# Kernel optimization log

Hardware: AMD Instinct MI355X
Metric: run time of the kernel (lower is better)

## Reference

```python
import jax, jax.numpy as jnp
import numpy as np

N = 50000          # nodes
E = 400000         # edges
MUL = 32           # multiplicity per irrep
NUM_NEIGHBORS = 8.0
INV_SQRT3 = 1.0 / np.sqrt(3.0)  # w3j(1,1,0) coefficient


def setup_inputs() -> dict:
    key = jax.random.key(0)
    ks = jax.random.split(key, 20)
    inp = {
        # node_input: 32x0e (dim 32) + 32x1o (dim 96) = 128
        "node_input": jax.random.normal(ks[0], (N, 4 * MUL), jnp.float32),
        "node_attr": jnp.ones((N, 1), jnp.float32),           # 1x0e trivial attr
        "edge_src": jax.random.randint(ks[1], (E,), 0, N, jnp.int32),
        "edge_dst": jax.random.randint(ks[2], (E,), 0, N, jnp.int32),
        "edge_attr": jax.random.normal(ks[3], (E, 4), jnp.float32),   # 1x0e + 1x1o
        "edge_scalars": jax.random.normal(ks[4], (E, 16), jnp.float32),
        # FullyConnectedTensorProduct weights (uvw, node_attr has mul 1)
        "w_sc0": jax.random.normal(ks[5], (MUL, MUL), jnp.float32),
        "w_sc1": jax.random.normal(ks[6], (MUL, MUL), jnp.float32),
        "w_lin1_0": jax.random.normal(ks[7], (MUL, MUL), jnp.float32),
        "w_lin1_1": jax.random.normal(ks[8], (MUL, MUL), jnp.float32),
        # radial FC net -> per-edge TP weights (numel = 4*MUL = 128)
        "fc_w1": jax.random.normal(ks[9], (16, 64), jnp.float32),
        "fc_w2": jax.random.normal(ks[10], (64, 4 * MUL), jnp.float32),
        # lin2: irreps_mid (64x0e+64x1o) x attr -> output
        "w_lin2_0": jax.random.normal(ks[11], (2 * MUL, MUL), jnp.float32),
        "w_lin2_1": jax.random.normal(ks[12], (2 * MUL, MUL), jnp.float32),
        # alpha: irreps_mid x attr -> 0e (zero-init in original; small randn for a nontrivial test)
        "w_alpha": 0.1 * jax.random.normal(ks[13], (2 * MUL, 1), jnp.float32),
        # sc_edges: irreps_mid x edge_attr -> edge_attr
        "w_se0a": jax.random.normal(ks[14], (2 * MUL,), jnp.float32),  # mid0e x ea0e -> 0e
        "w_se0b": jax.random.normal(ks[15], (2 * MUL,), jnp.float32),  # mid1o x ea1o -> 0e
        "w_se1a": jax.random.normal(ks[16], (2 * MUL,), jnp.float32),  # mid0e x ea1o -> 1o
        "w_se1b": jax.random.normal(ks[17], (2 * MUL,), jnp.float32),  # mid1o x ea0e -> 1o
    }
    return inp


def reference(node_input, node_attr, edge_src, edge_dst, edge_attr, edge_scalars,
              w_sc0, w_sc1, w_lin1_0, w_lin1_1, fc_w1, fc_w2,
              w_lin2_0, w_lin2_1, w_alpha, w_se0a, w_se0b, w_se1a, w_se1b):
    inv_nn = 1.0 / jnp.sqrt(jnp.asarray(NUM_NEIGHBORS, node_input.dtype))
    n = node_input.shape[0]
    x0 = node_input[:, :MUL]                       # (N, 32)   32x0e
    x1 = node_input[:, MUL:].reshape(n, MUL, 3)    # (N, 32, 3) 32x1o
    a = node_attr                                  # (N, 1)
    s_in = 1.0 / np.sqrt(MUL)                      # FCTP fan-in normalization

    # self-connection: FCTP(input, attr) -> output
    sc0 = (x0 @ w_sc0) * a * s_in
    sc1 = jnp.einsum('num,uw->nwm', x1, w_sc1) * a[:, :, None] * s_in
    node_self = jnp.concatenate([sc0, sc1.reshape(n, 3 * MUL)], axis=1)  # (N, 128)

    # lin1: FCTP(input, attr) -> input irreps
    f0 = (x0 @ w_lin1_0) * a * s_in
    f1 = jnp.einsum('num,uw->nwm', x1, w_lin1_1) * a[:, :, None] * s_in

    # gather source node features per edge
    g0 = f0[edge_src]                              # (E, 32)
    g1 = f1[edge_src]                              # (E, 32, 3)
    ea0 = edge_attr[:, :1]                         # (E, 1)   1x0e
    ea1 = edge_attr[:, 1:]                         # (E, 3)   1x1o

    # radial net -> per-edge TP weights (FullyConnectedNet with sin activation)
    h = jnp.sin(edge_scalars @ fc_w1 * (1.0 / np.sqrt(16.0)))
    w = h @ fc_w2 * (1.0 / np.sqrt(64.0))          # (E, 128)
    wA, wB, wC, wD = jnp.split(w, 4, axis=1)       # each (E, 32)

    # uvu tensor product, 4 instructions
    mA = wA * g0 * ea0                                           # 0e x 0e -> 0e
    mD = wD * jnp.einsum('eum,em->eu', g1, ea1) * INV_SQRT3      # 1o x 1o -> 0e
    mB = (wB * g0)[:, :, None] * ea1[:, None, :]                 # 0e x 1o -> 1o
    mC = (wC[:, :, None] * g1) * ea0[:, :, None]                 # 1o x 0e -> 1o
    mid0 = jnp.concatenate([mA, mD], axis=1)       # (E, 64)  64x0e
    mid1 = jnp.concatenate([mB, mC], axis=1)       # (E, 64, 3) 64x1o

    # scatter-add to destination nodes
    n0 = jax.ops.segment_sum(mid0, edge_dst, num_segments=n) * inv_nn
    n1 = jax.ops.segment_sum(mid1, edge_dst, num_segments=n) * inv_nn

    s_mid = 1.0 / np.sqrt(2 * MUL)
    out0 = (n0 @ w_lin2_0) * a * s_mid
    out1 = jnp.einsum('num,uw->nwm', n1, w_lin2_1) * a[:, :, None] * s_mid
    node_conv = jnp.concatenate([out0, out1.reshape(n, 3 * MUL)], axis=1)

    # alpha gate (sc.output_mask is all ones here, so alpha = 1 - 1 + alpha*1)
    alpha = (n0 @ w_alpha) * a * s_mid             # (N, 1)
    node_conv_out = node_self + alpha * node_conv  # (N, 128)

    # sc_edges: FCTP(mid, edge_attr) -> edge_attr irreps; fan-in = 128 per output
    s_se = 1.0 / np.sqrt(4 * MUL)
    se0 = ((mid0 @ w_se0a) * ea0[:, 0]
           + jnp.einsum('eum,em,u->e', mid1, ea1, w_se0b) * INV_SQRT3) * s_se
    se1 = ((mid0 @ w_se1a)[:, None] * ea1
           + jnp.einsum('eum,u->em', mid1, w_se1b) * ea0) * s_se
    edge_conv_out = edge_attr + jnp.concatenate([se0[:, None], se1], axis=1) * inv_nn

    return node_conv_out, edge_conv_out
```

## Files before the change

kernel.cpp:

```cpp
#include <hip/hip_runtime.h>
#include <math.h>

#define N_NODES 50000
#define E_EDGES 400000
#define NPRE_BLOCKS 6250
#define NHIST_BLOCKS 1563
#define NEDGE_BLOCKS 6250

typedef _Float16 f16x2 __attribute__((ext_vector_type(2)));
typedef _Float16 f16x4 __attribute__((ext_vector_type(4)));
typedef _Float16 f16x8 __attribute__((ext_vector_type(8)));
typedef float    f32x4 __attribute__((ext_vector_type(4)));

static constexpr float S_IN      = 0.17677669529663687f;
static constexpr float S_MID     = 0.125f;
static constexpr float S_SE      = 0.08838834764831843f;
static constexpr float INV_NN    = 0.35355339059327373f;
static constexpr float INV_SQRT3 = 0.5773502691896258f;
static constexpr float FC1_S     = 0.25f;
static constexpr float FC2_S     = 0.125f;

#define BAR_LDS() asm volatile("s_waitcnt lgkmcnt(0)\n\ts_barrier" ::: "memory")

__device__ inline float wave_reduce_dpp(float v) {
    int x;
    x = __builtin_amdgcn_update_dpp(0, __float_as_int(v), 0x111, 0xf, 0xf, true); v += __int_as_float(x);
    x = __builtin_amdgcn_update_dpp(0, __float_as_int(v), 0x112, 0xf, 0xf, true); v += __int_as_float(x);
    x = __builtin_amdgcn_update_dpp(0, __float_as_int(v), 0x114, 0xf, 0xf, true); v += __int_as_float(x);
    x = __builtin_amdgcn_update_dpp(0, __float_as_int(v), 0x118, 0xf, 0xf, true); v += __int_as_float(x);
    x = __builtin_amdgcn_update_dpp(0, __float_as_int(v), 0x142, 0xa, 0xf, true); v += __int_as_float(x);
    x = __builtin_amdgcn_update_dpp(0, __float_as_int(v), 0x143, 0xc, 0xf, true); v += __int_as_float(x);
    return __int_as_float(__builtin_amdgcn_readlane(__float_as_int(v), 63));
}

__global__ __launch_bounds__(256) void pre_hist_kernel(
    const float* __restrict__ node_input, const float* __restrict__ node_attr,
    const float* __restrict__ w_sc0, const float* __restrict__ w_sc1,
    const float* __restrict__ w_lin1_0, const float* __restrict__ w_lin1_1,
    float* __restrict__ out_self, _Float16* __restrict__ ws_h,
    const int* __restrict__ edge_dst, int* __restrict__ counts,
    const float* __restrict__ edge_scalars, _Float16* __restrict__ ES_h,
    float* __restrict__ nacc)
{
    const int t = threadIdx.x;
    if (blockIdx.x >= NPRE_BLOCKS) {
        const int e = (blockIdx.x - NPRE_BLOCKS) * 256 + t;
        if (e < E_EDGES) {
            atomicAdd(&counts[edge_dst[e]], 1);
            const float4* s4 = (const float4*)edge_scalars + (size_t)e * 4;
            _Float16* dp = ES_h + (size_t)e * 16;
            #pragma unroll
            for (int i = 0; i < 4; ++i) {
                const float4 v = s4[i];
                f16x4 p = {(_Float16)v.x, (_Float16)v.y, (_Float16)v.z, (_Float16)v.w};
                *(f16x4*)&dp[i * 4] = p;
            }
        }
        return;
    }
    const int n0 = blockIdx.x * 8;
    __shared__ __align__(16) float sx[8 * 128];
    __shared__ float sa[8];
    {
        const int k = t >> 5, q = t & 31;
        const float4 v = ((const float4*)(node_input + (size_t)n0 * 128))[t];
        if (q < 8) {
            *(float4*)&sx[k * 128 + q * 4] = v;
        } else {
            const int base = q * 4 - 32;
            const float vv[4] = {v.x, v.y, v.z, v.w};
            #pragma unroll
            for (int j = 0; j < 4; ++j) {
                const int uj = (base + j) / 3, mj = (base + j) % 3;
                sx[k * 128 + 32 + mj * 32 + uj] = vv[j];
            }
        }
    }
    {
        float4* nz = (float4*)(nacc + (size_t)n0 * 256);
        const float4 z4 = {0.f, 0.f, 0.f, 0.f};
        nz[t] = z4; nz[t + 256] = z4;
    }
    if (t < 8) sa[t] = node_attr[n0 + t];
    __syncthreads();

    const int half = t >> 7;
    const int idx  = t & 127;
    float wcol[32];
    int m = 0, xoff = 0;
    if (idx < 32) {
        const float* __restrict__ W = half ? w_lin1_0 : w_sc0;
        #pragma unroll
        for (int u = 0; u < 32; ++u) wcol[u] = W[u * 32 + idx];
    } else {
        const float* __restrict__ W = half ? w_lin1_1 : w_sc1;
        const int j = idx - 32;
        const int w = j / 3; m = j % 3;
        xoff = 32 + m * 32;
        #pragma unroll
        for (int u = 0; u < 32; ++u) wcol[u] = W[u * 32 + w];
    }
    #pragma unroll
    for (int k = 0; k < 8; ++k) {
        const float* xb = sx + k * 128 + xoff;
        float acc = 0.f;
        #pragma unroll
        for (int u4 = 0; u4 < 8; ++u4) {
            const f32x4 xv = *(const f32x4*)&xb[u4 * 4];
            acc += xv[0] * wcol[u4 * 4 + 0];
            acc += xv[1] * wcol[u4 * 4 + 1];
            acc += xv[2] * wcol[u4 * 4 + 2];
            acc += xv[3] * wcol[u4 * 4 + 3];
        }
        const float v = acc * sa[k] * S_IN;
        if (half) ws_h[(size_t)(n0 + k) * 128 + idx] = (_Float16)v;
        else      out_self[(size_t)(n0 + k) * 128 + idx] = v;
    }
}

__global__ __launch_bounds__(1024) void scan_block_kernel(
    const int* __restrict__ counts, int* __restrict__ cursor, int* __restrict__ bsum,
    const float* __restrict__ fc_w1, const float* __restrict__ fc_w2,
    const float* __restrict__ w_se0a, const float* __restrict__ w_se0b,
    const float* __restrict__ w_se1a, const float* __restrict__ w_se1b,
    _Float16* __restrict__ W2T_g, _Float16* __restrict__ W1T_g,
    _Float16* __restrict__ BT_g)
{
    const int t = threadIdx.x;
    if (blockIdx.x == 49) {
        for (int u = t; u < 8192; u += 1024) {
            const int k = u >> 7, c = u & 127;
            W2T_g[c * 72 + k] = (_Float16)fc_w2[u];
        }
        {
            W2T_g[(t >> 3) * 72 + 64 + (t & 7)] = (_Float16)0.f;
        }
        {
            const int j = t >> 4, k = t & 15;
            W1T_g[t] = (_Float16)fc_w1[k * 64 + j];
        }
        for (int u = t; u < 2112; u += 1024) BT_g[u] = (_Float16)0.f;
        __syncthreads();
        if (t < 256) {
            const int uu = t & 63, p = t >> 6;
            const float ev = (p == 0) ? w_se0a[uu] : w_se1b[uu];
            const float ov = (p == 0) ? w_se1a[uu] : w_se0b[uu];
            BT_g[(2 * p) * 264 + 4 * uu + p]     = (_Float16)ev;
            BT_g[(2 * p + 1) * 264 + 4 * uu + p] = (_Float16)ov;
        }
        return;
    }
    const int idx = blockIdx.x * 1024 + t;
    const int c   = (idx < N_NODES) ? counts[idx] : 0;
    int v = c, x;
    x = __builtin_amdgcn_update_dpp(0, v, 0x111, 0xf, 0xf, true); v += x;
    x = __builtin_amdgcn_update_dpp(0, v, 0x112, 0xf, 0xf, true); v += x;
    x = __builtin_amdgcn_update_dpp(0, v, 0x114, 0xf, 0xf, true); v += x;
    x = __builtin_amdgcn_update_dpp(0, v, 0x118, 0xf, 0xf, true); v += x;
    x = __builtin_amdgcn_update_dpp(0, v, 0x142, 0xa, 0xf, true); v += x;
    x = __builtin_amdgcn_update_dpp(0, v, 0x143, 0xc, 0xf, true); v += x;
    __shared__ int swv[16], sex[16];
    const int wid = t >> 6;
    if ((t & 63) == 63) swv[wid] = v;
    __syncthreads();
    if (t < 16) {
        int a = 0;
        for (int j = 0; j < t; ++j) a += swv[j];
        sex[t] = a;
        if (t == 15) bsum[blockIdx.x] = a + swv[15];
    }
    __syncthreads();
    if (idx < N_NODES) cursor[idx] = v - c + sex[wid];
}

__global__ __launch_bounds__(1024) void scan_fixup_kernel(
    int* __restrict__ cursor, const int* __restrict__ bsum)
{
    __shared__ int boff_s;
    const int t = threadIdx.x;
    if (t < 64) {
        int v = (t < (int)blockIdx.x) ? bsum[t] : 0;
        #pragma unroll
        for (int off = 32; off >= 1; off >>= 1) v += __shfl_down(v, off, 64);
        if (t == 0) boff_s = v;
    }
    __syncthreads();
    const int idx = blockIdx.x * 1024 + t;
    if (idx < N_NODES) cursor[idx] += boff_s;
}

__global__ __launch_bounds__(256) void scatter_kernel(
    const int* __restrict__ edge_dst, int* __restrict__ cursor,
    int* __restrict__ sorted_eid)
{
    const int e = blockIdx.x * 256 + threadIdx.x;
    if (e < E_EDGES) {
        const int p = atomicAdd(&cursor[edge_dst[e]], 1);
        sorted_eid[p] = e;
    }
}

__global__ __launch_bounds__(256, 5) void edge_kernel(
    const _Float16* __restrict__ ws_h,
    const int* __restrict__ edge_src, const int* __restrict__ edge_dst,
    const float* __restrict__ edge_attr, const _Float16* __restrict__ ES_h,
    const _Float16* __restrict__ W2T_g, const _Float16* __restrict__ W1T_g,
    const _Float16* __restrict__ BT_g,
    const int* __restrict__ sorted_eid,
    float* __restrict__ nacc, float* __restrict__ edge_out)
{
    __shared__ __align__(16) _Float16 sArena[15040];
    __shared__ __align__(16) float sEA[64 * 4];
    __shared__ __align__(16) float sDep[4][36];
    __shared__ int sSRC[64];
    __shared__ int sDST[64];
    __shared__ int sEID[64];

    _Float16* __restrict__ sW2T  = sArena;
    _Float16* __restrict__ sHT   = sArena + 9216;
    _Float16* __restrict__ sWt   = sArena;
    _Float16* __restrict__ sMidA = sArena + 8704;
    _Float16* __restrict__ sBT   = sArena + 12928;

    const int t    = threadIdx.x;
    const int lane = t & 63;
    const int wv   = t >> 6;
    const int quad = lane >> 4;
    const int mm   = lane & 15;

    const int orig = blockIdx.x;
    const int xcd  = orig & 7;
    constexpr int q = NEDGE_BLOCKS >> 3, r = NEDGE_BLOCKS & 7;
    const int bid = (xcd < r ? xcd * (q + 1) : r * (q + 1) + (xcd - r) * q) + (orig >> 3);
    const int e0 = bid * 64;
    const int eb = wv * 16;

    f16x8 a_w1[4];
    f16x8 b_es = {};
    if (quad < 2) {
        const int myeid = sorted_eid[e0 + eb + mm];
        b_es = *(const f16x8*)&ES_h[(size_t)myeid * 16 + quad * 8];
        #pragma unroll
        for (int jt = 0; jt < 4; ++jt)
            a_w1[jt] = *(const f16x8*)&W1T_g[(jt * 16 + mm) * 16 + quad * 8];
    } else {
        #pragma unroll
        for (int jt = 0; jt < 4; ++jt) a_w1[jt] = (f16x8){};
    }

    for (int i = t; i < 1152; i += 256)
        ((f16x8*)sW2T)[i] = ((const f16x8*)W2T_g)[i];
    if (t < 64) {
        const int eid = sorted_eid[e0 + t];
        *(float4*)&sEA[t * 4] = ((const float4*)edge_attr)[eid];
        sEID[t] = eid;
    } else if (t < 128) {
        sSRC[t - 64] = edge_src[sorted_eid[e0 + (t - 64)]];
    } else if (t < 192) {
        sDST[t - 128] = edge_dst[sorted_eid[e0 + (t - 128)]];
    }
    BAR_LDS();

    const bool hi = lane >= 32;
    const int  u  = lane - 32;
    const int idxA = hi ? (32 + 3 * u) : lane;
    const int idxB = hi ? (33 + 3 * u) : lane;
    const int idxC = hi ? (34 + 3 * u) : lane;
    const int col1 = hi ? (96 + u) : lane;
    const int col2 = hi ? (64 + u) : (32 + lane);

    float ga[4][4], gb[4][4], gc[4][4];
    #pragma unroll
    for (int b = 0; b < 4; ++b)
        #pragma unroll
        for (int i = 0; i < 4; ++i) {
            const _Float16* fr = ws_h + (size_t)sSRC[eb + b * 4 + i] * 128;
            ga[b][i] = (float)fr[idxA];
            gb[b][i] = (float)fr[idxB];
            gc[b][i] = (float)fr[idxC];
        }
    asm volatile("" ::: "memory");

    #pragma unroll
    for (int jt = 0; jt < 4; ++jt) {
        f32x4 d = {0.f, 0.f, 0.f, 0.f};
        d = __builtin_amdgcn_mfma_f32_16x16x32_f16(a_w1[jt], b_es, d, 0, 0, 0);
        f16x4 hv;
        hv[0] = (_Float16)__sinf(d[0] * FC1_S);
        hv[1] = (_Float16)__sinf(d[1] * FC1_S);
        hv[2] = (_Float16)__sinf(d[2] * FC1_S);
        hv[3] = (_Float16)__sinf(d[3] * FC1_S);
        *(f16x4*)&sHT[(eb + mm) * 72 + jt * 16 + quad * 4] = hv;
    }
    BAR_LDS();

    f32x4 dacc[8];
    {
        const f16x8 b_lo = *(const f16x8*)&sHT[(eb + mm) * 72 + quad * 8];
        const f16x8 b_hi = *(const f16x8*)&sHT[(eb + mm) * 72 + 32 + quad * 8];
        #pragma unroll
        for (int ct = 0; ct < 8; ++ct) {
            const f16x8 a_lo = *(const f16x8*)&sW2T[(ct * 16 + mm) * 72 + quad * 8];
            const f16x8 a_hi = *(const f16x8*)&sW2T[(ct * 16 + mm) * 72 + 32 + quad * 8];
            f32x4 d = {0.f, 0.f, 0.f, 0.f};
            d = __builtin_amdgcn_mfma_f32_16x16x32_f16(a_lo, b_lo, d, 0, 0, 0);
            d = __builtin_amdgcn_mfma_f32_16x16x32_f16(a_hi, b_hi, d, 0, 0, 0);
            dacc[ct] = d;
        }
    }
    BAR_LDS();

    {
        #pragma unroll
        for (int ct = 0; ct < 8; ++ct) {
            f16x4 v;
            v[0] = (_Float16)(dacc[ct][0] * FC2_S);
            v[1] = (_Float16)(dacc[ct][1] * FC2_S);
            v[2] = (_Float16)(dacc[ct][2] * FC2_S);
            v[3] = (_Float16)(dacc[ct][3] * FC2_S);
            *(f16x4*)&sWt[(eb + mm) * 136 + ct * 16 + quad * 4] = v;
        }
        for (int i = t; i < 264; i += 256)
            ((f16x8*)sBT)[i] = ((const f16x8*)BT_g)[i];
    }
    BAR_LDS();

    float w1f[16], w2f[16];
    #pragma unroll
    for (int e = 0; e < 16; ++e) {
        w1f[e] = (float)sWt[(eb + e) * 136 + col1];
        w2f[e] = (float)sWt[(eb + e) * 136 + col2];
    }

    int   cur = -1;
    float am0 = 0.f, axx = 0.f, ayy = 0.f, azz = 0.f;
    _Float16* __restrict__ myA = sMidA + wv * 1056;
    const _Float16* __restrict__ arow = myA + (mm & 3) * 264;
    const _Float16* __restrict__ brow = sBT + (mm & 7) * 264;

    #pragma unroll
    for (int b = 0; b < 4; ++b) {
        #pragma unroll
        for (int i = 0; i < 4; ++i) {
            const int el  = eb + b * 4 + i;
            const int dst = sDST[el];
            const float ea0 = sEA[el * 4 + 0];
            const float e1x = sEA[el * 4 + 1];
            const float e1y = sEA[el * 4 + 2];
            const float e1z = sEA[el * 4 + 3];
            const float w1v = w1f[b * 4 + i];
            const float w2v = w2f[b * 4 + i];

            float mid0, m1x, m1y, m1z;
            if (!hi) {
                mid0 = w1v * ga[b][i] * ea0;
                const float wbg = w2v * ga[b][i];
                m1x = wbg * e1x; m1y = wbg * e1y; m1z = wbg * e1z;
            } else {
                const float dot = ga[b][i] * e1x + gb[b][i] * e1y + gc[b][i] * e1z;
                mid0 = w1v * dot * INV_SQRT3;
                const float wce = w2v * ea0;
                m1x = wce * ga[b][i]; m1y = wce * gb[b][i]; m1z = wce * gc[b][i];
            }

            if (dst != cur) {
                if (cur >= 0) {
                    float* np_ = nacc + (size_t)cur * 256;
                    atomicAdd(np_ + lane, am0);
                    atomicAdd(np_ + 64 + lane, axx);
                    atomicAdd(np_ + 128 + lane, ayy);
                    atomicAdd(np_ + 192 + lane, azz);
                }
                cur = dst; am0 = axx = ayy = azz = 0.f;
            }
            am0 += mid0; axx += m1x; ayy += m1y; azz += m1z;

            f16x4 mv;
            mv[0] = (_Float16)mid0; mv[1] = (_Float16)m1x;
            mv[2] = (_Float16)m1y;  mv[3] = (_Float16)m1z;
            *(f16x4*)&myA[i * 264 + 4 * lane] = mv;
        }

        f32x4 d = {0.f, 0.f, 0.f, 0.f};
        #pragma unroll
        for (int ks = 0; ks < 8; ++ks) {
            const f16x8 a  = *(const f16x8*)&arow[ks * 32 + quad * 8];
            const f16x8 bb = *(const f16x8*)&brow[ks * 32 + quad * 8];
            d = __builtin_amdgcn_mfma_f32_16x16x32_f16(a, bb, d, 0, 0, 0);
        }
        if (lane < 8) {
            float4 f4; f4.x = d[0]; f4.y = d[1]; f4.z = d[2]; f4.w = d[3];
            *(float4*)&sDep[wv][lane * 4] = f4;
        }
        if (lane < 4) {
            const int el = eb + b * 4 + lane;
            const float c0 = sDep[wv][ 0 + lane], c1 = sDep[wv][ 4 + lane];
            const float c2 = sDep[wv][ 8 + lane], c3 = sDep[wv][12 + lane];
            const float c4 = sDep[wv][16 + lane], c5 = sDep[wv][20 + lane];
            const float c6 = sDep[wv][24 + lane], c7 = sDep[wv][28 + lane];
            const float ea0 = sEA[el * 4 + 0];
            const float e1x = sEA[el * 4 + 1];
            const float e1y = sEA[el * 4 + 2];
            const float e1z = sEA[el * 4 + 3];
            const float s0 = c0 * ea0 + (c3 * e1x + c5 * e1y + c7 * e1z) * INV_SQRT3;
            float4 o;
            o.x = ea0 + s0 * S_SE * INV_NN;
            o.y = e1x + (c1 * e1x + c2 * ea0) * S_SE * INV_NN;
            o.z = e1y + (c1 * e1y + c4 * ea0) * S_SE * INV_NN;
            o.w = e1z + (c1 * e1z + c6 * ea0) * S_SE * INV_NN;
            *(float4*)&edge_out[(size_t)sEID[el] * 4] = o;
        }
    }
    if (cur >= 0) {
        float* np_ = nacc + (size_t)cur * 256;
        atomicAdd(np_ + lane, am0);
        atomicAdd(np_ + 64 + lane, axx);
        atomicAdd(np_ + 128 + lane, ayy);
        atomicAdd(np_ + 192 + lane, azz);
    }
}

__global__ __launch_bounds__(128) void node_post_kernel(
    const float* __restrict__ nacc, const float* __restrict__ node_attr,
    const float* __restrict__ w_lin2_0, const float* __restrict__ w_lin2_1,
    const float* __restrict__ w_alpha, float* __restrict__ out)
{
    const int n0 = blockIdx.x * 8, t = threadIdx.x;
    __shared__ __align__(16) float sn[8 * 256];
    __shared__ float salpha[8];
    const float4* src = (const float4*)(nacc + (size_t)n0 * 256);
    #pragma unroll
    for (int i = 0; i < 4; ++i) ((float4*)sn)[t + i * 128] = src[t + i * 128];
    __syncthreads();

    if (t < 64) {
        const float wa = w_alpha[t];
        #pragma unroll
        for (int k = 0; k < 8; ++k) {
            const float r = wave_reduce_dpp(sn[k * 256 + t] * wa);
            if (t == 0) salpha[k] = r;
        }
    }
    __syncthreads();

    float wcol[64];
    int xoff = 0;
    if (t < 32) {
        #pragma unroll
        for (int u = 0; u < 64; ++u) wcol[u] = w_lin2_0[u * 32 + t];
    } else {
        const int j = t - 32; const int w = j / 3; const int m = j % 3;
        xoff = 64 + m * 64;
        #pragma unroll
        for (int u = 0; u < 64; ++u) wcol[u] = w_lin2_1[u * 32 + w];
    }
    #pragma unroll
    for (int k = 0; k < 8; ++k) {
        const float* xb = sn + k * 256 + xoff;
        float acc = 0.f;
        #pragma unroll
        for (int u4 = 0; u4 < 16; ++u4) {
            const f32x4 xv = *(const f32x4*)&xb[u4 * 4];
            acc += xv[0] * wcol[u4 * 4 + 0];
            acc += xv[1] * wcol[u4 * 4 + 1];
            acc += xv[2] * wcol[u4 * 4 + 2];
            acc += xv[3] * wcol[u4 * 4 + 3];
        }
        const float a  = node_attr[n0 + k];
        const float sc = a * S_MID * INV_NN;
        const size_t o = (size_t)(n0 + k) * 128 + t;
        out[o] = out[o] + (salpha[k] * sc) * (acc * sc);
    }
}

extern "C" void kernel_launch(void* const* d_in, const int* in_sizes, int n_in,
                              void* d_out, int out_size, void* d_ws, size_t ws_size,
                              hipStream_t stream)
{
    const float* node_input   = (const float*)d_in[0];
    const float* node_attr    = (const float*)d_in[1];
    const int*   edge_src     = (const int*)d_in[2];
    const int*   edge_dst     = (const int*)d_in[3];
    const float* edge_attr    = (const float*)d_in[4];
    const float* edge_scalars = (const float*)d_in[5];
    const float* w_sc0        = (const float*)d_in[6];
    const float* w_sc1        = (const float*)d_in[7];
    const float* w_lin1_0     = (const float*)d_in[8];
    const float* w_lin1_1     = (const float*)d_in[9];
    const float* fc_w1        = (const float*)d_in[10];
    const float* fc_w2        = (const float*)d_in[11];
    const float* w_lin2_0     = (const float*)d_in[12];
    const float* w_lin2_1     = (const float*)d_in[13];
    const float* w_alpha      = (const float*)d_in[14];
    const float* w_se0a       = (const float*)d_in[15];
    const float* w_se0b       = (const float*)d_in[16];
    const float* w_se1a       = (const float*)d_in[17];
    const float* w_se1b       = (const float*)d_in[18];

    float* out      = (float*)d_out;
    float* edge_out = out + (size_t)N_NODES * 128;

    _Float16* ws_h = (_Float16*)d_ws;
    _Float16* ES_h = ws_h + (size_t)N_NODES * 128;
    float* nacc   = (float*)((char*)d_ws + (size_t)N_NODES * 128 * 4);
    int*   counts = (int*)(nacc + (size_t)N_NODES * 256);
    int*   cursor = counts + N_NODES;
    int*   sid    = cursor + N_NODES;
    int*   bsum   = sid + E_EDGES;
    _Float16* W2T_g = (_Float16*)(bsum + 64);
    _Float16* W1T_g = W2T_g + 9216;
    _Float16* BT_g  = W1T_g + 1024;

    hipMemsetAsync(counts, 0, N_NODES * sizeof(int), stream);

    pre_hist_kernel<<<NPRE_BLOCKS + NHIST_BLOCKS, 256, 0, stream>>>(
        node_input, node_attr, w_sc0, w_sc1, w_lin1_0, w_lin1_1, out, ws_h,
        edge_dst, counts, edge_scalars, ES_h, nacc);

    scan_block_kernel<<<50, 1024, 0, stream>>>(counts, cursor, bsum,
        fc_w1, fc_w2, w_se0a, w_se0b, w_se1a, w_se1b, W2T_g, W1T_g, BT_g);
    scan_fixup_kernel<<<49, 1024, 0, stream>>>(cursor, bsum);
    scatter_kernel<<<(E_EDGES + 255) / 256, 256, 0, stream>>>(edge_dst, cursor, sid);

    edge_kernel<<<NEDGE_BLOCKS, 256, 0, stream>>>(
        ws_h, edge_src, edge_dst, edge_attr, ES_h, W2T_g, W1T_g, BT_g,
        sid, nacc, edge_out);

    node_post_kernel<<<N_NODES / 8, 128, 0, stream>>>(
        nacc, node_attr, w_lin2_0, w_lin2_1, w_alpha, out);
}
```

Before: 386.7 us.

## Make edge kernel wave-independent: drop block barriers, load weights from global

The edge kernel no longer stages W2T and BT in shared memory behind block-wide barriers. Each wave now loads its own edge metadata and reads the small weight matrices straight from global/L2 into registers. Shared memory is laid out so waves never overlap, so block barriers become per-wave LDS waitcnt fences. This trades extra register pressure and global loads for the removal of block synchronisation, and lowers the occupancy hint from 5 to 4 waves.

```diff
diff --git a/kernel.cpp b/kernel.cpp
--- a/kernel.cpp
+++ b/kernel.cpp
@@ -20,7 +20,7 @@
 static constexpr float FC1_S     = 0.25f;
 static constexpr float FC2_S     = 0.125f;
 
-#define BAR_LDS() asm volatile("s_waitcnt lgkmcnt(0)\n\ts_barrier" ::: "memory")
+#define WAVE_LDS_FENCE() asm volatile("s_waitcnt lgkmcnt(0)" ::: "memory")
 
 __device__ inline float wave_reduce_dpp(float v) {
     int x;
@@ -87,7 +87,7 @@
     const int half = t >> 7;
     const int idx  = t & 127;
     float wcol[32];
-    int m = 0, xoff = 0;
+    int xoff = 0;
     if (idx < 32) {
         const float* __restrict__ W = half ? w_lin1_0 : w_sc0;
         #pragma unroll
@@ -95,7 +95,7 @@
     } else {
         const float* __restrict__ W = half ? w_lin1_1 : w_sc1;
         const int j = idx - 32;
-        const int w = j / 3; m = j % 3;
+        const int w = j / 3; const int m = j % 3;
         xoff = 32 + m * 32;
         #pragma unroll
         for (int u = 0; u < 32; ++u) wcol[u] = W[u * 32 + w];
@@ -200,7 +200,7 @@
     }
 }
 
-__global__ __launch_bounds__(256, 5) void edge_kernel(
+__global__ __launch_bounds__(256, 4) void edge_kernel(
     const _Float16* __restrict__ ws_h,
     const int* __restrict__ edge_src, const int* __restrict__ edge_dst,
     const float* __restrict__ edge_attr, const _Float16* __restrict__ ES_h,
@@ -209,18 +209,16 @@
     const int* __restrict__ sorted_eid,
     float* __restrict__ nacc, float* __restrict__ edge_out)
 {
-    __shared__ __align__(16) _Float16 sArena[15040];
+    __shared__ __align__(16) _Float16 sArena[17536];
     __shared__ __align__(16) float sEA[64 * 4];
     __shared__ __align__(16) float sDep[4][36];
     __shared__ int sSRC[64];
     __shared__ int sDST[64];
     __shared__ int sEID[64];
 
-    _Float16* __restrict__ sW2T  = sArena;
-    _Float16* __restrict__ sHT   = sArena + 9216;
-    _Float16* __restrict__ sWt   = sArena;
-    _Float16* __restrict__ sMidA = sArena + 8704;
-    _Float16* __restrict__ sBT   = sArena + 12928;
+    _Float16* __restrict__ sHT   = sArena;
+    _Float16* __restrict__ sWt   = sArena + 4608;
+    _Float16* __restrict__ sMidA = sArena + 13312;
 
     const int t    = threadIdx.x;
     const int lane = t & 63;
@@ -247,19 +245,19 @@
         #pragma unroll
         for (int jt = 0; jt < 4; ++jt) a_w1[jt] = (f16x8){};
     }
-
-    for (int i = t; i < 1152; i += 256)
-        ((f16x8*)sW2T)[i] = ((const f16x8*)W2T_g)[i];
-    if (t < 64) {
-        const int eid = sorted_eid[e0 + t];
-        *(float4*)&sEA[t * 4] = ((const float4*)edge_attr)[eid];
-        sEID[t] = eid;
-    } else if (t < 128) {
-        sSRC[t - 64] = edge_src[sorted_eid[e0 + (t - 64)]];
-    } else if (t < 192) {
-        sDST[t - 128] = edge_dst[sorted_eid[e0 + (t - 128)]];
-    }
-    BAR_LDS();
+    f16x8 bt[8];
+    #pragma unroll
+    for (int ks = 0; ks < 8; ++ks)
+        bt[ks] = *(const f16x8*)&BT_g[(mm & 7) * 264 + ks * 32 + quad * 8];
+
+    if (lane < 16) {
+        const int eid = sorted_eid[e0 + eb + lane];
+        sEID[eb + lane] = eid;
+        sSRC[eb + lane] = edge_src[eid];
+        sDST[eb + lane] = edge_dst[eid];
+        *(float4*)&sEA[(eb + lane) * 4] = ((const float4*)edge_attr)[eid];
+    }
+    WAVE_LDS_FENCE();
 
     const bool hi = lane >= 32;
     const int  u  = lane - 32;
@@ -292,7 +290,7 @@
         hv[3] = (_Float16)__sinf(d[3] * FC1_S);
         *(f16x4*)&sHT[(eb + mm) * 72 + jt * 16 + quad * 4] = hv;
     }
-    BAR_LDS();
+    WAVE_LDS_FENCE();
 
     f32x4 dacc[8];
     {
@@ -300,46 +298,39 @@
         const f16x8 b_hi = *(const f16x8*)&sHT[(eb + mm) * 72 + 32 + quad * 8];
         #pragma unroll
         for (int ct = 0; ct < 8; ++ct) {
-            const f16x8 a_lo = *(const f16x8*)&sW2T[(ct * 16 + mm) * 72 + quad * 8];
-            const f16x8 a_hi = *(const f16x8*)&sW2T[(ct * 16 + mm) * 72 + 32 + quad * 8];
+            const f16x8 a_lo = *(const f16x8*)&W2T_g[(ct * 16 + mm) * 72 + quad * 8];
+            const f16x8 a_hi = *(const f16x8*)&W2T_g[(ct * 16 + mm) * 72 + 32 + quad * 8];
             f32x4 d = {0.f, 0.f, 0.f, 0.f};
             d = __builtin_amdgcn_mfma_f32_16x16x32_f16(a_lo, b_lo, d, 0, 0, 0);
             d = __builtin_amdgcn_mfma_f32_16x16x32_f16(a_hi, b_hi, d, 0, 0, 0);
             dacc[ct] = d;
         }
     }
-    BAR_LDS();
-
-    {
-        #pragma unroll
-        for (int ct = 0; ct < 8; ++ct) {
-            f16x4 v;
-            v[0] = (_Float16)(dacc[ct][0] * FC2_S);
-            v[1] = (_Float16)(dacc[ct][1] * FC2_S);
-            v[2] = (_Float16)(dacc[ct][2] * FC2_S);
-            v[3] = (_Float16)(dacc[ct][3] * FC2_S);
-            *(f16x4*)&sWt[(eb + mm) * 136 + ct * 16 + quad * 4] = v;
-        }
-        for (int i = t; i < 264; i += 256)
-            ((f16x8*)sBT)[i] = ((const f16x8*)BT_g)[i];
-    }
-    BAR_LDS();
-
-    float w1f[16], w2f[16];
-    #pragma unroll
-    for (int e = 0; e < 16; ++e) {
-        w1f[e] = (float)sWt[(eb + e) * 136 + col1];
-        w2f[e] = (float)sWt[(eb + e) * 136 + col2];
-    }
+
+    #pragma unroll
+    for (int ct = 0; ct < 8; ++ct) {
+        f16x4 v;
+        v[0] = (_Float16)(dacc[ct][0] * FC2_S);
+        v[1] = (_Float16)(dacc[ct][1] * FC2_S);
+        v[2] = (_Float16)(dacc[ct][2] * FC2_S);
+        v[3] = (_Float16)(dacc[ct][3] * FC2_S);
+        *(f16x4*)&sWt[(eb + mm) * 136 + ct * 16 + quad * 4] = v;
+    }
+    WAVE_LDS_FENCE();
 
     int   cur = -1;
     float am0 = 0.f, axx = 0.f, ayy = 0.f, azz = 0.f;
     _Float16* __restrict__ myA = sMidA + wv * 1056;
     const _Float16* __restrict__ arow = myA + (mm & 3) * 264;
-    const _Float16* __restrict__ brow = sBT + (mm & 7) * 264;
 
     #pragma unroll
     for (int b = 0; b < 4; ++b) {
+        float w1b[4], w2b[4];
+        #pragma unroll
+        for (int i = 0; i < 4; ++i) {
+            w1b[i] = (float)sWt[(eb + b * 4 + i) * 136 + col1];
+            w2b[i] = (float)sWt[(eb + b * 4 + i) * 136 + col2];
+        }
         #pragma unroll
         for (int i = 0; i < 4; ++i) {
             const int el  = eb + b * 4 + i;
@@ -348,8 +339,8 @@
             const float e1x = sEA[el * 4 + 1];
             const float e1y = sEA[el * 4 + 2];
             const float e1z = sEA[el * 4 + 3];
-            const float w1v = w1f[b * 4 + i];
-            const float w2v = w2f[b * 4 + i];
+            const float w1v = w1b[i];
+            const float w2v = w2b[i];
 
             float mid0, m1x, m1y, m1z;
             if (!hi) {
@@ -384,9 +375,8 @@
         f32x4 d = {0.f, 0.f, 0.f, 0.f};
         #pragma unroll
         for (int ks = 0; ks < 8; ++ks) {
-            const f16x8 a  = *(const f16x8*)&arow[ks * 32 + quad * 8];
-            const f16x8 bb = *(const f16x8*)&brow[ks * 32 + quad * 8];
-            d = __builtin_amdgcn_mfma_f32_16x16x32_f16(a, bb, d, 0, 0, 0);
+            const f16x8 a = *(const f16x8*)&arow[ks * 32 + quad * 8];
+            d = __builtin_amdgcn_mfma_f32_16x16x32_f16(a, bt[ks], d, 0, 0, 0);
         }
         if (lane < 8) {
             float4 f4; f4.x = d[0]; f4.y = d[1]; f4.z = d[2]; f4.w = d[3];
```

After: 369.2 us. 1.05x faster.
